# Kernel tuning notes

Hardware: AMD Instinct MI355X
Metric: run time of the kernel (lower is better)

Reference implementation:

```python
import jax, jax.numpy as jnp
import numpy as np

NHEAD = 8

def setup_inputs() -> dict:
    key = jax.random.key(0)
    ks = jax.random.split(key, 7)
    B, N, D = 8, 1024, 512
    scale = 1.0 / np.sqrt(D)
    return {
        "x": jax.random.normal(ks[0], (B, N, D), dtype=jnp.float32),
        "graph_bias": jax.random.normal(ks[1], (B, N, N), dtype=jnp.float32),
        "in_proj_w": jax.random.normal(ks[2], (3 * D, D), dtype=jnp.float32) * scale,
        "in_proj_b": jax.random.normal(ks[3], (3 * D,), dtype=jnp.float32) * 0.02,
        "out_proj_w": jax.random.normal(ks[4], (D, D), dtype=jnp.float32) * scale,
        "out_proj_b": jax.random.normal(ks[5], (D,), dtype=jnp.float32) * 0.02,
        "bias_strength": jnp.ones((), dtype=jnp.float32),
    }

def reference(x, graph_bias, in_proj_w, in_proj_b, out_proj_w, out_proj_b, bias_strength):
    B, N, D = x.shape
    H = NHEAD
    hd = D // H
    # fused QKV projection (matches nn.MultiheadAttention in_proj)
    qkv = x @ in_proj_w.T + in_proj_b          # (B, N, 3D)
    q, k, v = jnp.split(qkv, 3, axis=-1)
    # (B, H, N, hd)
    q = q.reshape(B, N, H, hd).transpose(0, 2, 1, 3)
    k = k.reshape(B, N, H, hd).transpose(0, 2, 1, 3)
    v = v.reshape(B, N, H, hd).transpose(0, 2, 1, 3)
    # additive bias from predicted causal structure
    alpha = jax.nn.sigmoid(bias_strength)
    causal_mask = jax.nn.sigmoid(graph_bias).transpose(0, 2, 1)   # (B, N, N)
    causal_mask = alpha * causal_mask + (1.0 - alpha) * 0.5
    attn_bias = (causal_mask - 0.5) * 10.0                        # (B, N, N)
    scores = jnp.einsum("bhqd,bhkd->bhqk", q, k) / jnp.sqrt(jnp.asarray(hd, x.dtype))
    scores = scores + attn_bias[:, None, :, :]                    # broadcast over heads
    probs = jax.nn.softmax(scores, axis=-1)
    out = jnp.einsum("bhqk,bhkd->bhqd", probs, v)                 # (B, H, N, hd)
    out = out.transpose(0, 2, 1, 3).reshape(B, N, D)
    return out @ out_proj_w.T + out_proj_b
```

## Files before the change

kernel.cpp:

```cpp
#include <hip/hip_runtime.h>

typedef __attribute__((ext_vector_type(8))) __bf16 bf16x8;
typedef __attribute__((ext_vector_type(4))) __bf16 bf16x4;
typedef __attribute__((ext_vector_type(4))) float f32x4;
typedef __attribute__((ext_vector_type(8))) _Float16 f16x8;

#define LOG2E 1.44269504088896340736f

__device__ __forceinline__ void async_load16(const void* g, void* l) {
  __builtin_amdgcn_global_load_lds(
      (const __attribute__((address_space(1))) void*)g,
      (__attribute__((address_space(3))) void*)l, 16, 0, 0);
}

__device__ __forceinline__ float fast_exp2(float x) {
#if __has_builtin(__builtin_amdgcn_exp2f)
  return __builtin_amdgcn_exp2f(x);
#else
  return __expf(x * 0.6931471805599453f);
#endif
}

__global__ __launch_bounds__(256) void prep(
    const float* __restrict__ gbias, const float* __restrict__ bstr,
    _Float16* __restrict__ ebT,
    const float* __restrict__ a, __bf16* __restrict__ oa, int na4,
    const float* __restrict__ b2, __bf16* __restrict__ ob, int nb4,
    const float* __restrict__ c, __bf16* __restrict__ oc, int nc4) {
  if (blockIdx.x < 4096) {
    const int gid = blockIdx.x * 256 + threadIdx.x;
    const int lane = gid & 63;
    const int kt = (gid >> 6) & 31;
    const int qt = (gid >> 11) & 63;
    const int b = gid >> 17;
    const int g = lane >> 4, ln = lane & 15;
    const float alpha = 1.f / (1.f + __expf(-bstr[0]));
    const float bsc = 10.f * alpha * LOG2E;
    const float* base = gbias + (size_t)(b * 1024 + kt * 32 + ln) * 1024 + qt * 16 + g * 4;
    float4 va = *(const float4*)(base);
    float4 vb = *(const float4*)(base + 16 * 1024);
    float sv[8] = {va.x, va.y, va.z, va.w, vb.x, vb.y, vb.z, vb.w};
    f16x8 o;
#pragma unroll
    for (int i = 0; i < 8; ++i)
      o[i] = (_Float16)((1.f / (1.f + __expf(-sv[i])) - 0.5f) * bsc);
    *(f16x8*)(ebT + (size_t)gid * 8) = o;
  } else {
    int i = (blockIdx.x - 4096) * 256 + threadIdx.x;
    int n = na4 + nb4 + nc4;
    int stride = 2560 * 256;
    for (; i < n; i += stride) {
      const float4* s;
      bf16x4* d;
      int j;
      if (i < na4) { s = (const float4*)a; d = (bf16x4*)oa; j = i; }
      else if (i < na4 + nb4) { s = (const float4*)b2; d = (bf16x4*)ob; j = i - na4; }
      else { s = (const float4*)c; d = (bf16x4*)oc; j = i - na4 - nb4; }
      float4 v = s[j];
      bf16x4 o;
      o[0] = (__bf16)v.x; o[1] = (__bf16)v.y; o[2] = (__bf16)v.z; o[3] = (__bf16)v.w;
      d[j] = o;
    }
  }
}

template <int MODE>
__global__ __launch_bounds__(256) void gemm_bt(
    const __bf16* __restrict__ A, const __bf16* __restrict__ Bm,
    const float* __restrict__ bias, void* __restrict__ C0,
    __bf16* __restrict__ vT, int M, int N, int K, int nt) {
  __shared__ __align__(16) char smem[32768];
  char* lA = smem;
  char* lB = smem + 16384;
  const int t = threadIdx.x;
  const int lane = t & 63;
  const int wid = t >> 6;
  const int wm = wid >> 1, wn = wid & 1;
  const int g = lane >> 4, ln = lane & 15;
  const int qchunk = gridDim.x >> 3;
  const int wg = (blockIdx.x & 7) * qchunk + (blockIdx.x >> 3);
  const int m0 = (wg / nt) * 128;
  const int n0 = (wg % nt) * 128;

  const int srow = t >> 3;
  const int sswz = ((t & 7) * 16) ^ ((srow & 7) << 4);
  const size_t KB = (size_t)K * 2;
  const char* gA = (const char*)A + (size_t)m0 * KB;
  const char* gB = (const char*)Bm + (size_t)n0 * KB;

  f32x4 acc[4][4] = {};

  for (int k0 = 0; k0 < K; k0 += 64) {
    __syncthreads();
#pragma unroll
    for (int c = 0; c < 4; ++c) {
      int row = srow + 32 * c;
      async_load16(gA + (size_t)row * KB + k0 * 2 + sswz, lA + c * 4096 + t * 16);
      async_load16(gB + (size_t)row * KB + k0 * 2 + sswz, lB + c * 4096 + t * 16);
    }
    __syncthreads();
#pragma unroll
    for (int ks = 0; ks < 2; ++ks) {
      bf16x8 af[4], bf[4];
#pragma unroll
      for (int i = 0; i < 4; ++i) {
        int ar = wm * 64 + i * 16 + ln;
        int byo = (ks * 64 + g * 16) ^ ((ar & 7) << 4);
        af[i] = *(const bf16x8*)(lA + ar * 128 + byo);
        int br = wn * 64 + i * 16 + ln;
        bf[i] = *(const bf16x8*)(lB + br * 128 + byo);
      }
#pragma unroll
      for (int i = 0; i < 4; ++i)
#pragma unroll
        for (int j = 0; j < 4; ++j)
          acc[i][j] = __builtin_amdgcn_mfma_f32_16x16x32_bf16(af[i], bf[j], acc[i][j], 0, 0, 0);
    }
  }

#pragma unroll
  for (int j = 0; j < 4; ++j) {
    int col = n0 + wn * 64 + j * 16 + ln;
    float bv = bias[col];
    if (MODE == 0) {
#pragma unroll
      for (int i = 0; i < 4; ++i) {
        int row0 = m0 + wm * 64 + i * 16 + g * 4;
#pragma unroll
        for (int r = 0; r < 4; ++r)
          ((float*)C0)[(size_t)(row0 + r) * N + col] = acc[i][j][r] + bv;
      }
    } else if (col < 1024) {
      float scale = (col < 512) ? (0.125f * LOG2E) : 1.0f;
#pragma unroll
      for (int i = 0; i < 4; ++i) {
        int row0 = m0 + wm * 64 + i * 16 + g * 4;
#pragma unroll
        for (int r = 0; r < 4; ++r)
          ((__bf16*)C0)[(size_t)(row0 + r) * 1024 + col] = (__bf16)((acc[i][j][r] + bv) * scale);
      }
    } else {
      int h = (col - 1024) >> 6;
      int d = (col - 1024) & 63;
#pragma unroll
      for (int i = 0; i < 4; ++i) {
        int row0 = m0 + wm * 64 + i * 16 + g * 4;
        int b = row0 >> 10;
        bf16x4 pk;
#pragma unroll
        for (int r = 0; r < 4; ++r) pk[r] = (__bf16)(acc[i][j][r] + bv);
        *(bf16x4*)(vT + (((size_t)b * 8 + h) * 64 + d) * 1024 + (row0 & 1023)) = pk;
      }
    }
  }
}

__global__ __launch_bounds__(512, 4) void attn_fused(
    const __bf16* __restrict__ qk,
    const __bf16* __restrict__ vT,
    const _Float16* __restrict__ ebT,
    __bf16* __restrict__ attn) {
  __shared__ __align__(16) char smem[73728];
  const int t = threadIdx.x;
  const int lane = t & 63;
  const int wid = t >> 6;
  const int g = lane >> 4, ln = lane & 15;
  const int wg = ((blockIdx.x & 7) << 6) + (blockIdx.x >> 3);
  const int b = wg >> 6;
  const int rem = wg & 63;
  const int h = rem >> 3;
  const int qg = rem & 7;
  const int qt = qg * 8 + wid;
  const int q0 = qt << 4;

  char* Ps = smem + 65536 + wid * 1024;

  bf16x8 qf[2];
#pragma unroll
  for (int ks = 0; ks < 2; ++ks)
    qf[ks] = *(const bf16x8*)(qk + ((size_t)b * 1024 + q0 + ln) * 1024 +
                              h * 64 + ks * 32 + g * 8);

  float l_acc[4] = {0.f, 0.f, 0.f, 0.f};
  f32x4 o_acc[4] = {};

  const int krow = lane >> 3;
  const int ksrc = ((lane & 7) * 16) ^ (krow << 4);
  const int vrow = lane >> 2;
  const int vsrc = ((lane & 3) * 16) ^ ((vrow & 3) << 4);

  const char* qkb = (const char*)qk + (size_t)b * 1024 * 2048;
  const char* vTb = (const char*)vT + (size_t)(b * 8 + h) * 64 * 2048;
  const _Float16* ebp = ebT + (size_t)((b * 64 + qt) * 32) * 512 + lane * 8;

  auto stage = [&](int p, char* set) {
    if (wid < 4) {
#pragma unroll
      for (int j = 0; j < 4; ++j)
        async_load16(qkb + (size_t)((4 * p + j) * 32 + wid * 8 + krow) * 2048 +
                         1024 + h * 128 + ksrc,
                     set + j * 4096 + wid * 1024 + lane * 16);
    } else {
      int cc = wid - 4;
#pragma unroll
      for (int j = 0; j < 4; ++j)
        async_load16(vTb + (size_t)(cc * 16 + vrow) * 2048 + (size_t)(4 * p + j) * 64 + vsrc,
                     set + 16384 + j * 4096 + cc * 1024 + lane * 16);
    }
  };

  auto process = [&](const char* Kp, const char* Vp, f16x8 ebv) {
    bf16x8 kf[2][2];
#pragma unroll
    for (int ni = 0; ni < 2; ++ni) {
      int br = ni * 16 + ln;
      int sw = (br & 7) << 4;
#pragma unroll
      for (int ks = 0; ks < 2; ++ks)
        kf[ni][ks] = *(const bf16x8*)(Kp + br * 128 + ((ks * 64 + g * 16) ^ sw));
    }
    bf16x8 vf[4];
#pragma unroll
    for (int di = 0; di < 4; ++di)
      vf[di] = *(const bf16x8*)(Vp + (di * 16 + ln) * 64 + ((g * 16) ^ ((ln & 3) << 4)));

    f32x4 lbf0 = {(float)ebv[0], (float)ebv[1], (float)ebv[2], (float)ebv[3]};
    f32x4 lbf1 = {(float)ebv[4], (float)ebv[5], (float)ebv[6], (float)ebv[7]};
    f32x4 s[2];
    s[0] = __builtin_amdgcn_mfma_f32_16x16x32_bf16(qf[0], kf[0][0], lbf0, 0, 0, 0);
    s[0] = __builtin_amdgcn_mfma_f32_16x16x32_bf16(qf[1], kf[0][1], s[0], 0, 0, 0);
    s[1] = __builtin_amdgcn_mfma_f32_16x16x32_bf16(qf[0], kf[1][0], lbf1, 0, 0, 0);
    s[1] = __builtin_amdgcn_mfma_f32_16x16x32_bf16(qf[1], kf[1][1], s[1], 0, 0, 0);

#pragma unroll
    for (int r = 0; r < 4; ++r) {
      float p0 = fast_exp2(s[0][r]);
      float p1 = fast_exp2(s[1][r]);
      s[0][r] = p0; s[1][r] = p1;
      l_acc[r] += p0 + p1;
    }
#pragma unroll
    for (int ni = 0; ni < 2; ++ni)
#pragma unroll
      for (int r = 0; r < 4; ++r) {
        int q = g * 4 + r;
        *(__bf16*)(Ps + q * 64 + ((ni * 32 + ln * 2) ^ (((q >> 1) & 3) << 4))) =
            (__bf16)s[ni][r];
      }
    bf16x8 pf = *(const bf16x8*)(Ps + ln * 64 + ((g * 16) ^ (((ln >> 1) & 3) << 4)));

#pragma unroll
    for (int di = 0; di < 4; ++di)
      o_acc[di] = __builtin_amdgcn_mfma_f32_16x16x32_bf16(pf, vf[di], o_acc[di], 0, 0, 0);
  };

  stage(0, smem);
  f16x8 eb0 = *(const f16x8*)(ebp);
  f16x8 eb1 = *(const f16x8*)(ebp + 512);
  f16x8 eb2 = *(const f16x8*)(ebp + 1024);
  f16x8 eb3 = *(const f16x8*)(ebp + 1536);
  asm volatile("s_waitcnt vmcnt(0)" ::: "memory");
  __syncthreads();

  for (int p = 0; p < 8; ++p) {
    char* cur = smem + (p & 1) * 32768;
    char* nxt = smem + ((p + 1) & 1) * 32768;
    const int pn = (p + 1) & 7;

    stage(pn, nxt);
    f16x8 ebn0 = *(const f16x8*)(ebp + (size_t)(4 * pn) * 512);
    f16x8 ebn1 = *(const f16x8*)(ebp + (size_t)(4 * pn + 1) * 512);
    f16x8 ebn2 = *(const f16x8*)(ebp + (size_t)(4 * pn + 2) * 512);
    f16x8 ebn3 = *(const f16x8*)(ebp + (size_t)(4 * pn + 3) * 512);
    __builtin_amdgcn_sched_barrier(0);

    process(cur,         cur + 16384, eb0);
    process(cur + 4096,  cur + 20480, eb1);
    process(cur + 8192,  cur + 24576, eb2);
    process(cur + 12288, cur + 28672, eb3);

    asm volatile("s_waitcnt vmcnt(0)" ::: "memory");
    __builtin_amdgcn_sched_barrier(0);
    __syncthreads();
    eb0 = ebn0; eb1 = ebn1; eb2 = ebn2; eb3 = ebn3;
  }

#pragma unroll
  for (int r = 0; r < 4; ++r) {
    float rs = l_acc[r];
#pragma unroll
    for (int off = 1; off < 16; off <<= 1)
      rs += __shfl_xor(rs, off, 64);
    float inv = 1.f / rs;
    int q = q0 + g * 4 + r;
#pragma unroll
    for (int di = 0; di < 4; ++di)
      attn[((size_t)b * 1024 + q) * 512 + h * 64 + di * 16 + ln] =
          (__bf16)(o_acc[di][r] * inv);
  }
}

extern "C" void kernel_launch(void* const* d_in, const int* in_sizes, int n_in,
                              void* d_out, int out_size, void* d_ws, size_t ws_size,
                              hipStream_t stream) {
  const float* x     = (const float*)d_in[0];
  const float* gb    = (const float*)d_in[1];
  const float* w_in  = (const float*)d_in[2];
  const float* b_in  = (const float*)d_in[3];
  const float* w_out = (const float*)d_in[4];
  const float* b_out = (const float*)d_in[5];
  const float* bstr  = (const float*)d_in[6];

  char* ws = (char*)d_ws;
  __bf16* qk    = (__bf16*)(ws);
  __bf16* vT    = (__bf16*)(ws + 16777216);
  __bf16* xb    = (__bf16*)(ws + 25165824);
  __bf16* w1    = (__bf16*)(ws + 33554432);
  __bf16* w2    = (__bf16*)(ws + 35127296);
  _Float16* ebT = (_Float16*)(ws + 35651584);
  __bf16* attn_buf = xb;

  prep<<<6656, 256, 0, stream>>>(gb, bstr, ebT,
                                 x, xb, (8 * 1024 * 512) / 4,
                                 w_in, w1, (1536 * 512) / 4,
                                 w_out, w2, (512 * 512) / 4);

  gemm_bt<1><<<768, 256, 0, stream>>>(xb, w1, b_in, qk, vT, 8192, 1536, 512, 12);
  attn_fused<<<512, 512, 0, stream>>>(qk, vT, ebT, attn_buf);
  gemm_bt<0><<<256, 256, 0, stream>>>(attn_buf, w2, b_out, d_out, nullptr, 8192, 512, 512, 4);
}
```

Baseline: 89.75 us.

## Move graph-bias preprocessing into QKV GEMM launch, split bf16 conversion out

The graph-bias sigmoid/transposition work moves out of the prep kernel and into the QKV projection launch as extra blocks that run after the GEMM blocks. The bf16 conversions of x and the weights get their own small kernel. The aim is to overlap the memory-bound bias pass with the compute-bound GEMM instead of running it before the GEMM. In exchange, the GEMM's bf16 inputs must now come from a separate launch, and the GEMM and bias blocks compete for CUs.

```diff
diff --git a/kernel.cpp b/kernel.cpp
--- a/kernel.cpp
+++ b/kernel.cpp
@@ -21,14 +21,39 @@
 #endif
 }
 
-__global__ __launch_bounds__(256) void prep(
+__global__ void cvt3(const float* __restrict__ a, __bf16* __restrict__ oa, int na4,
+                     const float* __restrict__ b, __bf16* __restrict__ ob, int nb4,
+                     const float* __restrict__ c, __bf16* __restrict__ oc, int nc4) {
+  int i = blockIdx.x * blockDim.x + threadIdx.x;
+  int n = na4 + nb4 + nc4;
+  int stride = gridDim.x * blockDim.x;
+  for (; i < n; i += stride) {
+    const float4* s;
+    bf16x4* d;
+    int j;
+    if (i < na4) { s = (const float4*)a; d = (bf16x4*)oa; j = i; }
+    else if (i < na4 + nb4) { s = (const float4*)b; d = (bf16x4*)ob; j = i - na4; }
+    else { s = (const float4*)c; d = (bf16x4*)oc; j = i - na4 - nb4; }
+    float4 v = s[j];
+    bf16x4 o;
+    o[0] = (__bf16)v.x; o[1] = (__bf16)v.y; o[2] = (__bf16)v.z; o[3] = (__bf16)v.w;
+    d[j] = o;
+  }
+}
+
+__global__ __launch_bounds__(256) void gemm1_ebias(
+    const __bf16* __restrict__ A,
+    const __bf16* __restrict__ Bm,
+    const float* __restrict__ bias,
+    __bf16* __restrict__ qkO,
+    __bf16* __restrict__ vT,
     const float* __restrict__ gbias, const float* __restrict__ bstr,
-    _Float16* __restrict__ ebT,
-    const float* __restrict__ a, __bf16* __restrict__ oa, int na4,
-    const float* __restrict__ b2, __bf16* __restrict__ ob, int nb4,
-    const float* __restrict__ c, __bf16* __restrict__ oc, int nc4) {
-  if (blockIdx.x < 4096) {
-    const int gid = blockIdx.x * 256 + threadIdx.x;
+    _Float16* __restrict__ ebT) {
+  __shared__ __align__(16) char smem[32768];
+  const int t = threadIdx.x;
+
+  if (blockIdx.x >= 768) {
+    const int gid = (blockIdx.x - 768) * 256 + t;
     const int lane = gid & 63;
     const int kt = (gid >> 6) & 31;
     const int qt = (gid >> 11) & 63;
@@ -45,30 +70,88 @@
     for (int i = 0; i < 8; ++i)
       o[i] = (_Float16)((1.f / (1.f + __expf(-sv[i])) - 0.5f) * bsc);
     *(f16x8*)(ebT + (size_t)gid * 8) = o;
-  } else {
-    int i = (blockIdx.x - 4096) * 256 + threadIdx.x;
-    int n = na4 + nb4 + nc4;
-    int stride = 2560 * 256;
-    for (; i < n; i += stride) {
-      const float4* s;
-      bf16x4* d;
-      int j;
-      if (i < na4) { s = (const float4*)a; d = (bf16x4*)oa; j = i; }
-      else if (i < na4 + nb4) { s = (const float4*)b2; d = (bf16x4*)ob; j = i - na4; }
-      else { s = (const float4*)c; d = (bf16x4*)oc; j = i - na4 - nb4; }
-      float4 v = s[j];
-      bf16x4 o;
-      o[0] = (__bf16)v.x; o[1] = (__bf16)v.y; o[2] = (__bf16)v.z; o[3] = (__bf16)v.w;
-      d[j] = o;
-    }
-  }
-}
-
-template <int MODE>
-__global__ __launch_bounds__(256) void gemm_bt(
+    return;
+  }
+
+  char* lA = smem;
+  char* lB = smem + 16384;
+  const int lane = t & 63;
+  const int wid = t >> 6;
+  const int wm = wid >> 1, wn = wid & 1;
+  const int g = lane >> 4, ln = lane & 15;
+  const int wg = (blockIdx.x & 7) * 96 + (blockIdx.x >> 3);
+  const int m0 = (wg / 12) * 128;
+  const int n0 = (wg % 12) * 128;
+
+  const int srow = t >> 3;
+  const int sswz = ((t & 7) * 16) ^ ((srow & 7) << 4);
+  const size_t KB = 1024;
+  const char* gA = (const char*)A + (size_t)m0 * KB;
+  const char* gB = (const char*)Bm + (size_t)n0 * KB;
+
+  f32x4 acc[4][4] = {};
+
+  for (int k0 = 0; k0 < 512; k0 += 64) {
+    __syncthreads();
+#pragma unroll
+    for (int c = 0; c < 4; ++c) {
+      int row = srow + 32 * c;
+      async_load16(gA + (size_t)row * KB + k0 * 2 + sswz, lA + c * 4096 + t * 16);
+      async_load16(gB + (size_t)row * KB + k0 * 2 + sswz, lB + c * 4096 + t * 16);
+    }
+    __syncthreads();
+#pragma unroll
+    for (int ks = 0; ks < 2; ++ks) {
+      bf16x8 af[4], bf[4];
+#pragma unroll
+      for (int i = 0; i < 4; ++i) {
+        int ar = wm * 64 + i * 16 + ln;
+        int byo = (ks * 64 + g * 16) ^ ((ar & 7) << 4);
+        af[i] = *(const bf16x8*)(lA + ar * 128 + byo);
+        int br = wn * 64 + i * 16 + ln;
+        bf[i] = *(const bf16x8*)(lB + br * 128 + byo);
+      }
+#pragma unroll
+      for (int i = 0; i < 4; ++i)
+#pragma unroll
+        for (int j = 0; j < 4; ++j)
+          acc[i][j] = __builtin_amdgcn_mfma_f32_16x16x32_bf16(af[i], bf[j], acc[i][j], 0, 0, 0);
+    }
+  }
+
+#pragma unroll
+  for (int j = 0; j < 4; ++j) {
+    int col = n0 + wn * 64 + j * 16 + ln;
+    float bv = bias[col];
+    if (col < 1024) {
+      float scale = (col < 512) ? (0.125f * LOG2E) : 1.0f;
+#pragma unroll
+      for (int i = 0; i < 4; ++i) {
+        int row0 = m0 + wm * 64 + i * 16 + g * 4;
+#pragma unroll
+        for (int r = 0; r < 4; ++r)
+          qkO[(size_t)(row0 + r) * 1024 + col] = (__bf16)((acc[i][j][r] + bv) * scale);
+      }
+    } else {
+      int h = (col - 1024) >> 6;
+      int d = (col - 1024) & 63;
+#pragma unroll
+      for (int i = 0; i < 4; ++i) {
+        int row0 = m0 + wm * 64 + i * 16 + g * 4;
+        int b = row0 >> 10;
+        bf16x4 pk;
+#pragma unroll
+        for (int r = 0; r < 4; ++r) pk[r] = (__bf16)(acc[i][j][r] + bv);
+        *(bf16x4*)(vT + (((size_t)b * 8 + h) * 64 + d) * 1024 + (row0 & 1023)) = pk;
+      }
+    }
+  }
+}
+
+__global__ __launch_bounds__(256) void gemm_bt0(
     const __bf16* __restrict__ A, const __bf16* __restrict__ Bm,
-    const float* __restrict__ bias, void* __restrict__ C0,
-    __bf16* __restrict__ vT, int M, int N, int K, int nt) {
+    const float* __restrict__ bias, float* __restrict__ C0,
+    int M, int N, int K, int nt) {
   __shared__ __align__(16) char smem[32768];
   char* lA = smem;
   char* lB = smem + 16384;
@@ -122,35 +205,12 @@
   for (int j = 0; j < 4; ++j) {
     int col = n0 + wn * 64 + j * 16 + ln;
     float bv = bias[col];
-    if (MODE == 0) {
-#pragma unroll
-      for (int i = 0; i < 4; ++i) {
-        int row0 = m0 + wm * 64 + i * 16 + g * 4;
-#pragma unroll
-        for (int r = 0; r < 4; ++r)
-          ((float*)C0)[(size_t)(row0 + r) * N + col] = acc[i][j][r] + bv;
-      }
-    } else if (col < 1024) {
-      float scale = (col < 512) ? (0.125f * LOG2E) : 1.0f;
-#pragma unroll
-      for (int i = 0; i < 4; ++i) {
-        int row0 = m0 + wm * 64 + i * 16 + g * 4;
-#pragma unroll
-        for (int r = 0; r < 4; ++r)
-          ((__bf16*)C0)[(size_t)(row0 + r) * 1024 + col] = (__bf16)((acc[i][j][r] + bv) * scale);
-      }
-    } else {
-      int h = (col - 1024) >> 6;
-      int d = (col - 1024) & 63;
-#pragma unroll
-      for (int i = 0; i < 4; ++i) {
-        int row0 = m0 + wm * 64 + i * 16 + g * 4;
-        int b = row0 >> 10;
-        bf16x4 pk;
-#pragma unroll
-        for (int r = 0; r < 4; ++r) pk[r] = (__bf16)(acc[i][j][r] + bv);
-        *(bf16x4*)(vT + (((size_t)b * 8 + h) * 64 + d) * 1024 + (row0 & 1023)) = pk;
-      }
+#pragma unroll
+    for (int i = 0; i < 4; ++i) {
+      int row0 = m0 + wm * 64 + i * 16 + g * 4;
+#pragma unroll
+      for (int r = 0; r < 4; ++r)
+        C0[(size_t)(row0 + r) * N + col] = acc[i][j][r] + bv;
     }
   }
 }
@@ -320,12 +380,11 @@
   _Float16* ebT = (_Float16*)(ws + 35651584);
   __bf16* attn_buf = xb;
 
-  prep<<<6656, 256, 0, stream>>>(gb, bstr, ebT,
-                                 x, xb, (8 * 1024 * 512) / 4,
+  cvt3<<<2560, 256, 0, stream>>>(x, xb, (8 * 1024 * 512) / 4,
                                  w_in, w1, (1536 * 512) / 4,
                                  w_out, w2, (512 * 512) / 4);
 
-  gemm_bt<1><<<768, 256, 0, stream>>>(xb, w1, b_in, qk, vT, 8192, 1536, 512, 12);
+  gemm1_ebias<<<768 + 4096, 256, 0, stream>>>(xb, w1, b_in, qk, vT, gb, bstr, ebT);
   attn_fused<<<512, 512, 0, stream>>>(qk, vT, ebT, attn_buf);
-  gemm_bt<0><<<256, 256, 0, stream>>>(attn_buf, w2, b_out, d_out, nullptr, 8192, 512, 512, 4);
-}
+  gemm_bt0<<<256, 256, 0, stream>>>(attn_buf, w2, b_out, (float*)d_out, 8192, 512, 512, 4);
+}
```

New measurement: 82.35 us. 1.09x faster.
